# Kernel optimization log

Measured on AMD Instinct MI355X. Metric: run time of the kernel, lower is better.

## Reference

```python
import jax, jax.numpy as jnp
import numpy as np

B, L, DIM = 2, 1024, 512
HEADS = 8
D = DIM // HEADS
FORE_DIM, POST_DIM = 256, 1024
L_FORE, L_POST = 4 * L, L // 4


def setup_inputs() -> dict:
    key = jax.random.key(0)
    ks = jax.random.split(key, 8)
    s = 0.02  # weight init scale
    return {
        "x": jax.random.normal(ks[0], (B, L, DIM), jnp.float32),
        "fore_x": jax.random.normal(ks[1], (B, L_FORE, FORE_DIM), jnp.float32),
        "post_x": jax.random.normal(ks[2], (B, L_POST, POST_DIM), jnp.float32),
        # Linear weights stored [in, out] (transposed vs torch nn.Linear)
        "wq": jax.random.normal(ks[3], (DIM, DIM), jnp.float32) * s,
        "bq": jnp.zeros((DIM,), jnp.float32),
        "wkv1": jax.random.normal(ks[4], (FORE_DIM, 2 * DIM), jnp.float32) * s,
        "bkv1": jnp.zeros((2 * DIM,), jnp.float32),
        "wkv2": jax.random.normal(ks[5], (POST_DIM, 2 * DIM), jnp.float32) * s,
        "bkv2": jnp.zeros((2 * DIM,), jnp.float32),
        "wproj": jax.random.normal(ks[6], (3 * DIM, DIM), jnp.float32) * s,
        "bproj": jnp.zeros((DIM,), jnp.float32),
    }


def reference(x, fore_x, post_x, wq, bq, wkv1, bkv1, wkv2, bkv2, wproj, bproj):
    scale = D ** (-0.5)
    # q: [B, H, L, D], pre-scaled as in the torch code
    q = (x @ wq + bq).reshape(B, L, HEADS, D).transpose(0, 2, 1, 3) * scale

    def cross_attn(ctx, w, b):
        # ctx: [B, Lc, Cin] -> k, v: [B, H, Lc, D]
        kv = (ctx @ w + b).reshape(B, ctx.shape[1], 2, HEADS, D)
        k = kv[:, :, 0].transpose(0, 2, 1, 3)
        v = kv[:, :, 1].transpose(0, 2, 1, 3)
        attn = jax.nn.softmax(jnp.einsum("bhqd,bhkd->bhqk", q, k), axis=-1)
        out = jnp.einsum("bhqk,bhkd->bhqd", attn, v)
        return out.transpose(0, 2, 1, 3).reshape(B, L, DIM)

    x_2 = cross_attn(post_x, wkv2, bkv2)
    x_1 = cross_attn(fore_x, wkv1, bkv1)
    cat = jnp.concatenate([x, x_1, x_2], axis=2)  # [B, L, 3*DIM]
    return cat @ wproj + bproj
```

## Files before the change

### kernel.cpp

```cpp
#include <hip/hip_runtime.h>
#include <hip/hip_bf16.h>
#include <stdint.h>

typedef __attribute__((ext_vector_type(8))) short bf8;
typedef __attribute__((ext_vector_type(4))) short bf4;
typedef __attribute__((ext_vector_type(2))) short bf2;
typedef __attribute__((ext_vector_type(4))) float f32x4;

__device__ inline short f2bf(float f) {
  union { __hip_bfloat16 h; short s; } u;
  u.h = __float2bfloat16(f);
  return u.s;
}
__device__ inline float bf2f(short s) {
  union { short s; __hip_bfloat16 h; } u;
  u.s = s;
  return __bfloat162float(u.h);
}

__device__ inline f32x4 mfma16(bf8 a, bf8 b, f32x4 c) {
  return __builtin_amdgcn_mfma_f32_16x16x32_bf16(a, b, c, 0, 0, 0);
}

__global__ __launch_bounds__(256) void gemm3_k(
    const float* __restrict__ x, const float* __restrict__ fore,
    const float* __restrict__ post,
    const float* __restrict__ wq, const float* __restrict__ bq,
    const float* __restrict__ wkv1, const float* __restrict__ bkv1,
    const float* __restrict__ wkv2, const float* __restrict__ bkv2,
    short* __restrict__ qb, short* __restrict__ kv1, short* __restrict__ kv2,
    short* __restrict__ cat)
{
  __shared__ __align__(16) short a_lds[128 * 40];
  __shared__ __align__(16) short b_lds[64 * 40];

  const int bid = blockIdx.x;
  const float *A, *W, *bias;
  short* out;
  int K, N, lda, ldo, m0, n0, mode = 0;
  bool wcat = false;
  if (bid < 1024) {
    A = fore; W = wkv1; bias = bkv1; out = kv1;
    K = 256; N = 1024; lda = 256; ldo = 1024;
    m0 = (bid >> 4) * 128; n0 = (bid & 15) * 64;
  } else if (bid < 1152) {
    int j = bid - 1024;
    A = x; W = wq; bias = bq; out = qb;
    K = 512; N = 512; lda = 512; ldo = 512;
    m0 = (j >> 3) * 128; n0 = (j & 7) * 64;
    mode = 1; wcat = (j & 7) == 0;
  } else {
    int j = bid - 1152;
    A = post; W = wkv2; bias = bkv2; out = kv2;
    K = 1024; N = 1024; lda = 1024; ldo = 1024;
    m0 = (j >> 4) * 128; n0 = (j & 15) * 64;
  }

  const int tid = threadIdx.x;
  const int w = tid >> 6, lane = tid & 63, g = lane >> 4, lr = lane & 15;
  const int wrow = w & 1, wcol = w >> 1;

  f32x4 z = {0.f, 0.f, 0.f, 0.f};
  f32x4 acc[4][2];
#pragma unroll
  for (int mi = 0; mi < 4; ++mi)
#pragma unroll
    for (int ni = 0; ni < 2; ++ni) acc[mi][ni] = z;

  const int arow = tid >> 3, ac4 = tid & 7;
  const int bcol = tid & 63, bj4 = tid >> 6;

  float4 arf[4], arf_n[4];
  float wrg[8], wrg_n[8];

  auto LOADA = [&](int k0, float4* af, float* wg) {
#pragma unroll
    for (int i = 0; i < 4; ++i)
      af[i] = *(const float4*)&A[(size_t)(m0 + arow + 32 * i) * lda + k0 + ac4 * 4];
#pragma unroll
    for (int j = 0; j < 8; ++j)
      wg[j] = W[(size_t)(k0 + bj4 * 8 + j) * N + n0 + bcol];
  };

  LOADA(0, arf, wrg);

  for (int k0 = 0; k0 < K; k0 += 32) {
    __syncthreads();
    {
#pragma unroll
      for (int i = 0; i < 4; ++i) {
        int rr = arow + 32 * i;
        int s = (ac4 >> 1) ^ (rr & 3);
        bf4 o;
        o[0] = f2bf(arf[i].x); o[1] = f2bf(arf[i].y);
        o[2] = f2bf(arf[i].z); o[3] = f2bf(arf[i].w);
        *(bf4*)&a_lds[rr * 40 + s * 8 + (ac4 & 1) * 4] = o;
        if (wcat)
          *(bf4*)&cat[(size_t)(m0 + rr) * 1536 + k0 + ac4 * 4] = o;
      }
      int s = bj4 ^ (bcol & 3);
      bf8 o;
#pragma unroll
      for (int j = 0; j < 8; ++j) o[j] = f2bf(wrg[j]);
      *(bf8*)&b_lds[bcol * 40 + s * 8] = o;
    }
    if (k0 + 32 < K) LOADA(k0 + 32, arf_n, wrg_n);
    __syncthreads();

    bf8 afr[4], bfr[2];
#pragma unroll
    for (int mi = 0; mi < 4; ++mi) {
      int row = wrow * 64 + mi * 16 + lr;
      afr[mi] = *(const bf8*)&a_lds[row * 40 + ((g ^ (row & 3)) << 3)];
    }
#pragma unroll
    for (int ni = 0; ni < 2; ++ni) {
      int col = wcol * 32 + ni * 16 + lr;
      bfr[ni] = *(const bf8*)&b_lds[col * 40 + ((g ^ (col & 3)) << 3)];
    }
#pragma unroll
    for (int mi = 0; mi < 4; ++mi)
#pragma unroll
      for (int ni = 0; ni < 2; ++ni)
        acc[mi][ni] = mfma16(afr[mi], bfr[ni], acc[mi][ni]);

#pragma unroll
    for (int i = 0; i < 4; ++i) arf[i] = arf_n[i];
#pragma unroll
    for (int j = 0; j < 8; ++j) wrg[j] = wrg_n[j];
  }

#pragma unroll
  for (int ni = 0; ni < 2; ++ni) {
    int col = n0 + wcol * 32 + ni * 16 + lr;
    float bv = bias[col];
#pragma unroll
    for (int mi = 0; mi < 4; ++mi) {
      int rowb = m0 + wrow * 64 + mi * 16 + g * 4;
#pragma unroll
      for (int r = 0; r < 4; ++r) {
        float val = acc[mi][ni][r] + bv;
        if (mode == 1) val *= 0.125f;
        out[(size_t)(rowb + r) * ldo + col] = f2bf(val);
      }
    }
  }
}

__global__ __launch_bounds__(256) void gemmo_k(
    const short* __restrict__ A, const float* __restrict__ W,
    const float* __restrict__ bias, float* __restrict__ out,
    int N, int K, int lda, int ldo)
{
  __shared__ __align__(16) short a_lds[64 * 40];
  __shared__ __align__(16) short b_lds[64 * 40];
  const int tid = threadIdx.x;
  const int w = tid >> 6, lane = tid & 63, g = lane >> 4, lr = lane & 15;
  const int m0 = blockIdx.x * 64, n0 = blockIdx.y * 64;

  f32x4 z = {0.f, 0.f, 0.f, 0.f};
  f32x4 acc[4];
#pragma unroll
  for (int mi = 0; mi < 4; ++mi) acc[mi] = z;

  const int arow = tid >> 2, ac8 = tid & 3;
  const int bcol = tid & 63, bj4 = tid >> 6;
  bf8 arb, arb_n;
  float wrg[8], wrg_n[8];

  auto LOADA = [&](int k0, bf8& ab, float* wg) {
    ab = *(const bf8*)&A[(size_t)(m0 + arow) * lda + k0 + ac8 * 8];
#pragma unroll
    for (int j = 0; j < 8; ++j)
      wg[j] = W[(size_t)(k0 + bj4 * 8 + j) * N + n0 + bcol];
  };

  LOADA(0, arb, wrg);

  for (int k0 = 0; k0 < K; k0 += 32) {
    __syncthreads();
    *(bf8*)&a_lds[arow * 40 + ((ac8 ^ (arow & 3)) << 3)] = arb;
    {
      int s = bj4 ^ (bcol & 3);
      bf8 o;
#pragma unroll
      for (int j = 0; j < 8; ++j) o[j] = f2bf(wrg[j]);
      *(bf8*)&b_lds[bcol * 40 + s * 8] = o;
    }
    if (k0 + 32 < K) LOADA(k0 + 32, arb_n, wrg_n);
    __syncthreads();

    bf8 afr[4], bfr;
#pragma unroll
    for (int mi = 0; mi < 4; ++mi) {
      int row = mi * 16 + lr;
      afr[mi] = *(const bf8*)&a_lds[row * 40 + ((g ^ (row & 3)) << 3)];
    }
    {
      int col = w * 16 + lr;
      bfr = *(const bf8*)&b_lds[col * 40 + ((g ^ (col & 3)) << 3)];
    }
#pragma unroll
    for (int mi = 0; mi < 4; ++mi) acc[mi] = mfma16(afr[mi], bfr, acc[mi]);

    arb = arb_n;
#pragma unroll
    for (int j = 0; j < 8; ++j) wrg[j] = wrg_n[j];
  }

  {
    int col = n0 + w * 16 + lr;
    float bv = bias[col];
#pragma unroll
    for (int mi = 0; mi < 4; ++mi) {
      int rowb = m0 + mi * 16 + g * 4;
#pragma unroll
      for (int r = 0; r < 4; ++r)
        out[(size_t)(rowb + r) * ldo + col] = acc[mi][r] + bv;
    }
  }
}

__global__ __launch_bounds__(256) void attn_k(
    const short* __restrict__ q,
    const short* __restrict__ kv1, const short* __restrict__ kv2,
    short* __restrict__ o1, float* __restrict__ l1,
    short* __restrict__ o2, float* __restrict__ l2)
{
  __shared__ __align__(16) short k_lds[64 * 64];
  __shared__ __align__(16) short v_lds[64 * 72];
  const int tid = threadIdx.x;
  const int w = tid >> 6, lane = tid & 63, g = lane >> 4, lr = lane & 15;

  const int bid = blockIdx.x;
  const short* kvsrc;
  short* opart;
  float* lpart;
  int qt, h, bb, split, chunk, Lc;
  if (bid < 1024) {
    qt = bid & 7; h = (bid >> 3) & 7;
    int zz = bid >> 6; bb = zz >> 3; split = zz & 7;
    kvsrc = kv1; opart = o1; lpart = l1; chunk = 512; Lc = 4096;
  } else {
    int j = bid - 1024;
    qt = j & 7; h = (j >> 3) & 7;
    int zz = j >> 6; bb = zz >> 2; split = zz & 3;
    kvsrc = kv2; opart = o2; lpart = l2; chunk = 64; Lc = 256;
  }

  const int qbase = bb * 1024 + qt * 128 + w * 32;
  bf8 qfA[2], qfB[2];
#pragma unroll
  for (int s2 = 0; s2 < 2; ++s2) {
    const short* qp = &q[(size_t)(qbase + s2 * 16 + lr) * 512 + h * 64];
    qfA[s2] = *(const bf8*)&qp[g * 8];
    qfB[s2] = *(const bf8*)&qp[32 + g * 8];
  }

  const f32x4 z = {0.f, 0.f, 0.f, 0.f};
  f32x4 oaccT[2][4];
#pragma unroll
  for (int s2 = 0; s2 < 2; ++s2)
#pragma unroll
    for (int i = 0; i < 4; ++i) oaccT[s2][i] = z;
  float lsum_l[2] = {0.f, 0.f};

  const short* kvb = kvsrc + (size_t)bb * Lc * 1024 + (size_t)split * chunk * 1024;

  const int krow = tid >> 2, ksl = tid & 3;
  const short* kgp = kvb + (size_t)krow * 1024 + h * 64;
  const int vi = tid & 31, vj = tid >> 5;
  const short* vgp = kvb + (size_t)(2 * vi) * 1024 + 512 + h * 64 + vj * 8;
  const int lc0 = 2 * vi;
  const int vpos = (lc0 & 32) + ((lc0 & 12) << 1) + ((lc0 & 16) >> 2) + (lc0 & 3);

  bf8 k0c, k1c, v0c, v1c;
  k0c = *(const bf8*)(kgp + ksl * 8);
  k1c = *(const bf8*)(kgp + (ksl + 4) * 8);
  v0c = *(const bf8*)vgp;
  v1c = *(const bf8*)(vgp + 1024);

  const int nit = chunk >> 6;
  for (int it = 0; it < nit; ++it) {
    __syncthreads();
    *(bf8*)&k_lds[krow * 64 + ((ksl ^ (krow & 7)) << 3)] = k0c;
    *(bf8*)&k_lds[krow * 64 + (((ksl + 4) ^ (krow & 7)) << 3)] = k1c;
#pragma unroll
    for (int jj = 0; jj < 8; ++jj) {
      int d = vj * 8 + jj;
      bf2 pr; pr[0] = v0c[jj]; pr[1] = v1c[jj];
      *(bf2*)&v_lds[d * 72 + vpos] = pr;
    }
    __syncthreads();
    if (it + 1 < nit) {
      size_t off = (size_t)64 * 1024 * (it + 1);
      k0c = *(const bf8*)(kgp + off + ksl * 8);
      k1c = *(const bf8*)(kgp + off + (ksl + 4) * 8);
      v0c = *(const bf8*)(vgp + off);
      v1c = *(const bf8*)(vgp + off + 1024);
    }

    f32x4 sv[2][4];
#pragma unroll
    for (int t = 0; t < 4; ++t) {
      int lc = t * 16 + lr;
      bf8 kf0 = *(const bf8*)&k_lds[lc * 64 + ((g ^ (lc & 7)) << 3)];
      bf8 kf1 = *(const bf8*)&k_lds[lc * 64 + (((4 + g) ^ (lc & 7)) << 3)];
#pragma unroll
      for (int s2 = 0; s2 < 2; ++s2) {
        sv[s2][t] = mfma16(kf0, qfA[s2], z);
        sv[s2][t] = mfma16(kf1, qfB[s2], sv[s2][t]);
      }
    }

    bf8 pb[2][2];
#pragma unroll
    for (int s2 = 0; s2 < 2; ++s2) {
      float acc_l = 0.f;
#pragma unroll
      for (int t = 0; t < 4; ++t) {
        float p0 = __expf(sv[s2][t][0]);
        float p1 = __expf(sv[s2][t][1]);
        float p2 = __expf(sv[s2][t][2]);
        float p3 = __expf(sv[s2][t][3]);
        acc_l += (p0 + p1) + (p2 + p3);
        int c = t >> 1, hb = (t & 1) * 4;
        pb[s2][c][hb + 0] = f2bf(p0);
        pb[s2][c][hb + 1] = f2bf(p1);
        pb[s2][c][hb + 2] = f2bf(p2);
        pb[s2][c][hb + 3] = f2bf(p3);
      }
      lsum_l[s2] += acc_l;
    }

#pragma unroll
    for (int dt = 0; dt < 4; ++dt) {
      int d = dt * 16 + lr;
      bf8 vf0 = *(const bf8*)&v_lds[d * 72 + 8 * g];
      bf8 vf1 = *(const bf8*)&v_lds[d * 72 + 32 + 8 * g];
      oaccT[0][dt] = mfma16(vf0, pb[0][0], oaccT[0][dt]);
      oaccT[0][dt] = mfma16(vf1, pb[0][1], oaccT[0][dt]);
      oaccT[1][dt] = mfma16(vf0, pb[1][0], oaccT[1][dt]);
      oaccT[1][dt] = mfma16(vf1, pb[1][1], oaccT[1][dt]);
    }
  }

#pragma unroll
  for (int s2 = 0; s2 < 2; ++s2) {
    int prow = (bb * 8 + h) * 1024 + qt * 128 + w * 32 + s2 * 16 + lr;
    short* ob = opart + ((size_t)split * 16384 + prow) * 64;
#pragma unroll
    for (int dt = 0; dt < 4; ++dt) {
      bf4 o4;
#pragma unroll
      for (int r = 0; r < 4; ++r) o4[r] = f2bf(oaccT[s2][dt][r]);
      *(bf4*)&ob[dt * 16 + 4 * g] = o4;
    }
    float t = lsum_l[s2];
    t += __shfl_xor(t, 16);
    t += __shfl_xor(t, 32);
    if (g == 0) lpart[(size_t)split * 16384 + prow] = t;
  }
}

__global__ __launch_bounds__(256) void comb_k(
    const short* __restrict__ o1, const float* __restrict__ l1,
    const short* __restrict__ o2, const float* __restrict__ l2,
    short* __restrict__ cat)
{
  int row = blockIdx.x * 4 + (threadIdx.x >> 6);
  int d = threadIdx.x & 63;
  int bb = row >> 13, h = (row >> 10) & 7, qr = row & 1023;
  short* crow = &cat[(size_t)(bb * 1024 + qr) * 1536 + h * 64 + d];

  float o = 0.f, l = 0.f;
#pragma unroll
  for (int s = 0; s < 8; ++s) {
    o += bf2f(o1[((size_t)s * 16384 + row) * 64 + d]);
    l += l1[(size_t)s * 16384 + row];
  }
  crow[512] = f2bf(o / l);

  o = 0.f; l = 0.f;
#pragma unroll
  for (int s = 0; s < 4; ++s) {
    o += bf2f(o2[((size_t)s * 16384 + row) * 64 + d]);
    l += l2[(size_t)s * 16384 + row];
  }
  crow[1024] = f2bf(o / l);
}

extern "C" void kernel_launch(void* const* d_in, const int* in_sizes, int n_in,
                              void* d_out, int out_size, void* d_ws, size_t ws_size,
                              hipStream_t stream) {
  const float* x     = (const float*)d_in[0];
  const float* fore  = (const float*)d_in[1];
  const float* post  = (const float*)d_in[2];
  const float* wq    = (const float*)d_in[3];
  const float* bq    = (const float*)d_in[4];
  const float* wkv1  = (const float*)d_in[5];
  const float* bkv1  = (const float*)d_in[6];
  const float* wkv2  = (const float*)d_in[7];
  const float* bkv2  = (const float*)d_in[8];
  const float* wproj = (const float*)d_in[9];
  const float* bproj = (const float*)d_in[10];

  char* ws = (char*)d_ws;
  short* qb  = (short*)ws;
  short* kv1 = (short*)(ws + (2ull << 20));
  short* kv2 = (short*)(ws + (18ull << 20));
  short* cat = (short*)(ws + (19ull << 20));
  short* o1  = (short*)(ws + (25ull << 20));
  short* o2  = (short*)(ws + (41ull << 20));
  float* l1  = (float*)(ws + (49ull << 20));
  float* l2  = (float*)(ws + (50ull << 20));

  gemm3_k<<<1216, 256, 0, stream>>>(x, fore, post, wq, bq, wkv1, bkv1,
                                    wkv2, bkv2, qb, kv1, kv2, cat);
  attn_k<<<1536, 256, 0, stream>>>(qb, kv1, kv2, o1, l1, o2, l2);
  comb_k<<<4096, 256, 0, stream>>>(o1, l1, o2, l2, cat);
  gemmo_k<<<dim3(32, 8), 256, 0, stream>>>(cat, wproj, bproj, (float*)d_out,
                                           512, 1536, 1536, 512);
}
```

Before: 105.9 us.

## Split-K the q and kv2 projections, double-buffer LDS in GEMM kernels

```diff
diff --git a/kernel.cpp b/kernel.cpp
--- a/kernel.cpp
+++ b/kernel.cpp
@@ -25,35 +25,34 @@
 __global__ __launch_bounds__(256) void gemm3_k(
     const float* __restrict__ x, const float* __restrict__ fore,
     const float* __restrict__ post,
-    const float* __restrict__ wq, const float* __restrict__ bq,
-    const float* __restrict__ wkv1, const float* __restrict__ bkv1,
-    const float* __restrict__ wkv2, const float* __restrict__ bkv2,
-    short* __restrict__ qb, short* __restrict__ kv1, short* __restrict__ kv2,
-    short* __restrict__ cat)
+    const float* __restrict__ wq, const float* __restrict__ wkv1,
+    const float* __restrict__ bkv1, const float* __restrict__ wkv2,
+    short* __restrict__ kv1, short* __restrict__ cat,
+    float* __restrict__ qpart, float* __restrict__ kv2part)
 {
-  __shared__ __align__(16) short a_lds[128 * 40];
-  __shared__ __align__(16) short b_lds[64 * 40];
+  __shared__ __align__(16) short a_lds[2][128 * 40];
+  __shared__ __align__(16) short b_lds[2][64 * 40];
 
   const int bid = blockIdx.x;
-  const float *A, *W, *bias;
-  short* out;
-  int K, N, lda, ldo, m0, n0, mode = 0;
-  bool wcat = false;
+  const float *A, *W, *bias = nullptr;
+  void* out;
+  int N, lda, ldo, m0, n0, koff;
+  bool f32out, wcat = false;
   if (bid < 1024) {
     A = fore; W = wkv1; bias = bkv1; out = kv1;
-    K = 256; N = 1024; lda = 256; ldo = 1024;
-    m0 = (bid >> 4) * 128; n0 = (bid & 15) * 64;
-  } else if (bid < 1152) {
-    int j = bid - 1024;
-    A = x; W = wq; bias = bq; out = qb;
-    K = 512; N = 512; lda = 512; ldo = 512;
-    m0 = (j >> 3) * 128; n0 = (j & 7) * 64;
-    mode = 1; wcat = (j & 7) == 0;
+    N = 1024; lda = 256; ldo = 1024; koff = 0;
+    m0 = (bid >> 4) * 128; n0 = (bid & 15) * 64; f32out = false;
+  } else if (bid < 1280) {
+    int j = bid - 1024; int kc = j >> 7; j &= 127;
+    A = x; W = wq; out = qpart + (size_t)kc * (2048 * 512);
+    N = 512; lda = 512; ldo = 512; koff = kc * 256;
+    m0 = (j >> 3) * 128; n0 = (j & 7) * 64; f32out = true;
+    wcat = (j & 7) == 0;
   } else {
-    int j = bid - 1152;
-    A = post; W = wkv2; bias = bkv2; out = kv2;
-    K = 1024; N = 1024; lda = 1024; ldo = 1024;
-    m0 = (j >> 4) * 128; n0 = (j & 15) * 64;
+    int j = bid - 1280; int kc = j >> 6; j &= 63;
+    A = post; W = wkv2; out = kv2part + (size_t)kc * (512 * 1024);
+    N = 1024; lda = 1024; ldo = 1024; koff = kc * 256;
+    m0 = (j >> 4) * 128; n0 = (j & 15) * 64; f32out = true;
   }
 
   const int tid = threadIdx.x;
@@ -70,80 +69,116 @@
   const int arow = tid >> 3, ac4 = tid & 7;
   const int bcol = tid & 63, bj4 = tid >> 6;
 
-  float4 arf[4], arf_n[4];
-  float wrg[8], wrg_n[8];
-
-  auto LOADA = [&](int k0, float4* af, float* wg) {
+  float4 ra[4], rna[4];
+  float rw[8], rnw[8];
+
+  auto LOADA = [&](int kg, float4* af, float* wg) {
 #pragma unroll
     for (int i = 0; i < 4; ++i)
-      af[i] = *(const float4*)&A[(size_t)(m0 + arow + 32 * i) * lda + k0 + ac4 * 4];
+      af[i] = *(const float4*)&A[(size_t)(m0 + arow + 32 * i) * lda + kg + ac4 * 4];
 #pragma unroll
     for (int j = 0; j < 8; ++j)
-      wg[j] = W[(size_t)(k0 + bj4 * 8 + j) * N + n0 + bcol];
+      wg[j] = W[(size_t)(kg + bj4 * 8 + j) * N + n0 + bcol];
   };
-
-  LOADA(0, arf, wrg);
-
-  for (int k0 = 0; k0 < K; k0 += 32) {
-    __syncthreads();
-    {
-#pragma unroll
-      for (int i = 0; i < 4; ++i) {
-        int rr = arow + 32 * i;
-        int s = (ac4 >> 1) ^ (rr & 3);
-        bf4 o;
-        o[0] = f2bf(arf[i].x); o[1] = f2bf(arf[i].y);
-        o[2] = f2bf(arf[i].z); o[3] = f2bf(arf[i].w);
-        *(bf4*)&a_lds[rr * 40 + s * 8 + (ac4 & 1) * 4] = o;
-        if (wcat)
-          *(bf4*)&cat[(size_t)(m0 + rr) * 1536 + k0 + ac4 * 4] = o;
-      }
-      int s = bj4 ^ (bcol & 3);
-      bf8 o;
-#pragma unroll
-      for (int j = 0; j < 8; ++j) o[j] = f2bf(wrg[j]);
-      *(bf8*)&b_lds[bcol * 40 + s * 8] = o;
-    }
-    if (k0 + 32 < K) LOADA(k0 + 32, arf_n, wrg_n);
-    __syncthreads();
-
+  auto STAGE = [&](int b, const float4* af, const float* wg, int kg) {
+#pragma unroll
+    for (int i = 0; i < 4; ++i) {
+      int rr = arow + 32 * i;
+      int s = (ac4 >> 1) ^ (rr & 3);
+      bf4 o;
+      o[0] = f2bf(af[i].x); o[1] = f2bf(af[i].y);
+      o[2] = f2bf(af[i].z); o[3] = f2bf(af[i].w);
+      *(bf4*)&a_lds[b][rr * 40 + s * 8 + (ac4 & 1) * 4] = o;
+      if (wcat)
+        *(bf4*)&cat[(size_t)(m0 + rr) * 1536 + kg + ac4 * 4] = o;
+    }
+    int s = bj4 ^ (bcol & 3);
+    bf8 o;
+#pragma unroll
+    for (int j = 0; j < 8; ++j) o[j] = f2bf(wg[j]);
+    *(bf8*)&b_lds[b][bcol * 40 + s * 8] = o;
+  };
+
+  LOADA(koff, ra, rw);
+  STAGE(0, ra, rw, koff);
+  LOADA(koff + 32, rna, rnw);
+  __syncthreads();
+
+#pragma unroll
+  for (int it = 0; it < 8; ++it) {
+    if (it < 7) STAGE((it + 1) & 1, rna, rnw, koff + (it + 1) * 32);
+    if (it < 6) LOADA(koff + (it + 2) * 32, rna, rnw);
+
+    const int b = it & 1;
     bf8 afr[4], bfr[2];
 #pragma unroll
     for (int mi = 0; mi < 4; ++mi) {
       int row = wrow * 64 + mi * 16 + lr;
-      afr[mi] = *(const bf8*)&a_lds[row * 40 + ((g ^ (row & 3)) << 3)];
+      afr[mi] = *(const bf8*)&a_lds[b][row * 40 + ((g ^ (row & 3)) << 3)];
     }
 #pragma unroll
     for (int ni = 0; ni < 2; ++ni) {
       int col = wcol * 32 + ni * 16 + lr;
-      bfr[ni] = *(const bf8*)&b_lds[col * 40 + ((g ^ (col & 3)) << 3)];
+      bfr[ni] = *(const bf8*)&b_lds[b][col * 40 + ((g ^ (col & 3)) << 3)];
     }
 #pragma unroll
     for (int mi = 0; mi < 4; ++mi)
 #pragma unroll
       for (int ni = 0; ni < 2; ++ni)
         acc[mi][ni] = mfma16(afr[mi], bfr[ni], acc[mi][ni]);
-
-#pragma unroll
-    for (int i = 0; i < 4; ++i) arf[i] = arf_n[i];
-#pragma unroll
-    for (int j = 0; j < 8; ++j) wrg[j] = wrg_n[j];
+    __syncthreads();
   }
 
 #pragma unroll
   for (int ni = 0; ni < 2; ++ni) {
     int col = n0 + wcol * 32 + ni * 16 + lr;
-    float bv = bias[col];
+    float bv = f32out ? 0.f : bias[col];
 #pragma unroll
     for (int mi = 0; mi < 4; ++mi) {
       int rowb = m0 + wrow * 64 + mi * 16 + g * 4;
 #pragma unroll
       for (int r = 0; r < 4; ++r) {
         float val = acc[mi][ni][r] + bv;
-        if (mode == 1) val *= 0.125f;
-        out[(size_t)(rowb + r) * ldo + col] = f2bf(val);
+        if (f32out)
+          ((float*)out)[(size_t)(rowb + r) * ldo + col] = val;
+        else
+          ((short*)out)[(size_t)(rowb + r) * ldo + col] = f2bf(val);
       }
     }
+  }
+}
+
+__global__ __launch_bounds__(256) void finalize_k(
+    const float* __restrict__ qpart, const float* __restrict__ kv2part,
+    const float* __restrict__ bq, const float* __restrict__ bkv2,
+    short* __restrict__ qb, short* __restrict__ kv2)
+{
+  int i = blockIdx.x * 256 + threadIdx.x;
+  if (i < 262144) {
+    int col = (i * 4) & 511;
+    float4 a = ((const float4*)qpart)[i];
+    float4 b = ((const float4*)qpart)[i + 262144];
+    float4 bv = *(const float4*)&bq[col];
+    bf4 o;
+    o[0] = f2bf((a.x + b.x + bv.x) * 0.125f);
+    o[1] = f2bf((a.y + b.y + bv.y) * 0.125f);
+    o[2] = f2bf((a.z + b.z + bv.z) * 0.125f);
+    o[3] = f2bf((a.w + b.w + bv.w) * 0.125f);
+    ((bf4*)qb)[i] = o;
+  } else {
+    int j = i - 262144;
+    int col = (j * 4) & 1023;
+    float4 a = ((const float4*)kv2part)[j];
+    float4 b = ((const float4*)kv2part)[j + 131072];
+    float4 c = ((const float4*)kv2part)[j + 262144];
+    float4 d = ((const float4*)kv2part)[j + 393216];
+    float4 bv = *(const float4*)&bkv2[col];
+    bf4 o;
+    o[0] = f2bf(a.x + b.x + c.x + d.x + bv.x);
+    o[1] = f2bf(a.y + b.y + c.y + d.y + bv.y);
+    o[2] = f2bf(a.z + b.z + c.z + d.z + bv.z);
+    o[3] = f2bf(a.w + b.w + c.w + d.w + bv.w);
+    ((bf4*)kv2)[j] = o;
   }
 }
 
@@ -152,8 +187,8 @@
     const float* __restrict__ bias, float* __restrict__ out,
     int N, int K, int lda, int ldo)
 {
-  __shared__ __align__(16) short a_lds[64 * 40];
-  __shared__ __align__(16) short b_lds[64 * 40];
+  __shared__ __align__(16) short a_lds[2][64 * 40];
+  __shared__ __align__(16) short b_lds[2][64 * 40];
   const int tid = threadIdx.x;
   const int w = tid >> 6, lane = tid & 63, g = lane >> 4, lr = lane & 15;
   const int m0 = blockIdx.x * 64, n0 = blockIdx.y * 64;
@@ -165,47 +200,48 @@
 
   const int arow = tid >> 2, ac8 = tid & 3;
   const int bcol = tid & 63, bj4 = tid >> 6;
-  bf8 arb, arb_n;
-  float wrg[8], wrg_n[8];
-
-  auto LOADA = [&](int k0, bf8& ab, float* wg) {
-    ab = *(const bf8*)&A[(size_t)(m0 + arow) * lda + k0 + ac8 * 8];
+  bf8 ra, rna;
+  float rw[8], rnw[8];
+
+  auto LOADA = [&](int kg, bf8& ab, float* wg) {
+    ab = *(const bf8*)&A[(size_t)(m0 + arow) * lda + kg + ac8 * 8];
 #pragma unroll
     for (int j = 0; j < 8; ++j)
-      wg[j] = W[(size_t)(k0 + bj4 * 8 + j) * N + n0 + bcol];
+      wg[j] = W[(size_t)(kg + bj4 * 8 + j) * N + n0 + bcol];
   };
-
-  LOADA(0, arb, wrg);
-
-  for (int k0 = 0; k0 < K; k0 += 32) {
-    __syncthreads();
-    *(bf8*)&a_lds[arow * 40 + ((ac8 ^ (arow & 3)) << 3)] = arb;
-    {
-      int s = bj4 ^ (bcol & 3);
-      bf8 o;
-#pragma unroll
-      for (int j = 0; j < 8; ++j) o[j] = f2bf(wrg[j]);
-      *(bf8*)&b_lds[bcol * 40 + s * 8] = o;
-    }
-    if (k0 + 32 < K) LOADA(k0 + 32, arb_n, wrg_n);
-    __syncthreads();
-
+  auto STAGE = [&](int b, bf8 ab, const float* wg) {
+    *(bf8*)&a_lds[b][arow * 40 + ((ac8 ^ (arow & 3)) << 3)] = ab;
+    int s = bj4 ^ (bcol & 3);
+    bf8 o;
+#pragma unroll
+    for (int j = 0; j < 8; ++j) o[j] = f2bf(wg[j]);
+    *(bf8*)&b_lds[b][bcol * 40 + s * 8] = o;
+  };
+
+  const int nit = K >> 5;
+  LOADA(0, ra, rw);
+  STAGE(0, ra, rw);
+  LOADA(32, rna, rnw);
+  __syncthreads();
+
+  for (int it = 0; it < nit; ++it) {
+    if (it + 1 < nit) STAGE((it + 1) & 1, rna, rnw);
+    if (it + 2 < nit) LOADA((it + 2) * 32, rna, rnw);
+
+    const int b = it & 1;
     bf8 afr[4], bfr;
 #pragma unroll
     for (int mi = 0; mi < 4; ++mi) {
       int row = mi * 16 + lr;
-      afr[mi] = *(const bf8*)&a_lds[row * 40 + ((g ^ (row & 3)) << 3)];
+      afr[mi] = *(const bf8*)&a_lds[b][row * 40 + ((g ^ (row & 3)) << 3)];
     }
     {
       int col = w * 16 + lr;
-      bfr = *(const bf8*)&b_lds[col * 40 + ((g ^ (col & 3)) << 3)];
+      bfr = *(const bf8*)&b_lds[b][col * 40 + ((g ^ (col & 3)) << 3)];
     }
 #pragma unroll
     for (int mi = 0; mi < 4; ++mi) acc[mi] = mfma16(afr[mi], bfr, acc[mi]);
-
-    arb = arb_n;
-#pragma unroll
-    for (int j = 0; j < 8; ++j) wrg[j] = wrg_n[j];
+    __syncthreads();
   }
 
   {
@@ -406,17 +442,20 @@
   const float* bproj = (const float*)d_in[10];
 
   char* ws = (char*)d_ws;
-  short* qb  = (short*)ws;
-  short* kv1 = (short*)(ws + (2ull << 20));
-  short* kv2 = (short*)(ws + (18ull << 20));
-  short* cat = (short*)(ws + (19ull << 20));
-  short* o1  = (short*)(ws + (25ull << 20));
-  short* o2  = (short*)(ws + (41ull << 20));
-  float* l1  = (float*)(ws + (49ull << 20));
-  float* l2  = (float*)(ws + (50ull << 20));
-
-  gemm3_k<<<1216, 256, 0, stream>>>(x, fore, post, wq, bq, wkv1, bkv1,
-                                    wkv2, bkv2, qb, kv1, kv2, cat);
+  short* qb      = (short*)ws;
+  short* kv1     = (short*)(ws + (2ull << 20));
+  short* kv2     = (short*)(ws + (18ull << 20));
+  short* cat     = (short*)(ws + (19ull << 20));
+  short* o1      = (short*)(ws + (25ull << 20));
+  short* o2      = (short*)(ws + (41ull << 20));
+  float* l1      = (float*)(ws + (49ull << 20));
+  float* l2      = (float*)(ws + (50ull << 20));
+  float* qpart   = (float*)(ws + (51ull << 20));
+  float* kv2part = (float*)(ws + (59ull << 20));
+
+  gemm3_k<<<1536, 256, 0, stream>>>(x, fore, post, wq, wkv1, bkv1, wkv2,
+                                    kv1, cat, qpart, kv2part);
+  finalize_k<<<1536, 256, 0, stream>>>(qpart, kv2part, bq, bkv2, qb, kv2);
   attn_k<<<1536, 256, 0, stream>>>(qb, kv1, kv2, o1, l1, o2, l2);
   comb_k<<<4096, 256, 0, stream>>>(o1, l1, o2, l2, cat);
   gemmo_k<<<dim3(32, 8), 256, 0, stream>>>(cat, wproj, bproj, (float*)d_out,
```

Result: faster. 99.50 us (-6.1%).
